# Kernel optimization log

Hardware: AMD Instinct MI355X
Metric: run time of the kernel (lower is better)

The kernel has to match this reference:

```python
import jax, jax.numpy as jnp
import numpy as np

RESO = 64            # plane_resolution
PADDING = 0.1
HID = 128            # hidden_dim
CDIM = 128           # c_dim
NBLOCKS = 5
PLANES = ((0, 2), (0, 1), (1, 2))  # xz, xy, yz column picks


def _plane_index(p, cols):
    # normalize_coordinate + coordinate2index (2d)
    xy = p[..., list(cols)] / (1.0 + PADDING + 1e-3) + 0.5
    xy = jnp.clip(xy, 0.0, 1.0 - 1e-3)
    ij = (xy * RESO).astype(jnp.int32)
    return ij[..., 0] + RESO * ij[..., 1]  # [B, T]


def _flat_idx(idx, S):
    B = idx.shape[0]
    return (idx + jnp.arange(B, dtype=idx.dtype)[:, None] * S).reshape(-1)


def _scatter_max(src, idx, S):
    # src [B,T,F], idx [B,T] -> [B,S,F]; empty bins -> 0 (torch_scatter convention)
    B, T, F = src.shape
    m = jax.ops.segment_max(src.reshape(B * T, F), _flat_idx(idx, S), num_segments=B * S)
    m = jnp.where(jnp.isfinite(m), m, jnp.zeros((), src.dtype))
    return m.reshape(B, S, F)


def _scatter_mean(src, idx, S):
    B, T, F = src.shape
    flat = _flat_idx(idx, S)
    s = jax.ops.segment_sum(src.reshape(B * T, F), flat, num_segments=B * S)
    cnt = jax.ops.segment_sum(jnp.ones((B * T,), src.dtype), flat, num_segments=B * S)
    return (s / jnp.maximum(cnt, 1.0)[:, None]).reshape(B, S, F)


def _resblock(x, w0, b0, w1, b1, ws):
    # ONet ResnetBlockFC: fc_1(relu(fc_0(relu(x)))) + shortcut(x)
    net = jax.nn.relu(x) @ w0 + b0
    dx = jax.nn.relu(net) @ w1 + b1
    return x @ ws + dx


def setup_inputs() -> dict:
    key = jax.random.key(0)
    ks = jax.random.split(key, 10)
    sc = 0.05
    return {
        "p": jax.random.normal(ks[0], (8, 20000, 3), dtype=jnp.float32),
        "fc_pos_w": jax.random.normal(ks[1], (3, 2 * HID), dtype=jnp.float32) * sc,
        "fc_pos_b": jnp.zeros((2 * HID,), jnp.float32),
        "blk0_w": jax.random.normal(ks[2], (NBLOCKS, 2 * HID, HID), dtype=jnp.float32) * sc,
        "blk0_b": jnp.zeros((NBLOCKS, HID), jnp.float32),
        "blk1_w": jax.random.normal(ks[3], (NBLOCKS, HID, HID), dtype=jnp.float32) * sc,
        "blk1_b": jnp.zeros((NBLOCKS, HID), jnp.float32),
        "blk_sc_w": jax.random.normal(ks[4], (NBLOCKS, 2 * HID, HID), dtype=jnp.float32) * sc,
        "fc_c_w": jax.random.normal(ks[5], (HID, CDIM), dtype=jnp.float32) * sc,
        "fc_c_b": jnp.zeros((CDIM,), jnp.float32),
    }


def reference(p, fc_pos_w, fc_pos_b, blk0_w, blk0_b, blk1_w, blk1_b, blk_sc_w, fc_c_w, fc_c_b):
    S = RESO * RESO
    B = p.shape[0]
    idxs = [_plane_index(p, cols) for cols in PLANES]

    net = p @ fc_pos_w + fc_pos_b                         # [B,T,2H]
    net = _resblock(net, blk0_w[0], blk0_b[0], blk1_w[0], blk1_b[0], blk_sc_w[0])
    for i in range(1, NBLOCKS):
        pooled = jnp.zeros_like(net[..., :HID])
        for idx in idxs:
            fea = _scatter_max(net, idx, S)               # [B,S,H]
            pooled = pooled + jnp.take_along_axis(fea, idx[:, :, None], axis=1)
        net = jnp.concatenate([net, pooled], axis=-1)     # [B,T,2H]
        net = _resblock(net, blk0_w[i], blk0_b[i], blk1_w[i], blk1_b[i], blk_sc_w[i])

    c = net @ fc_c_w + fc_c_b                             # [B,T,C]
    feas = []
    for idx in idxs:
        fp = _scatter_mean(c, idx, S)                     # [B,S,C]
        feas.append(fp.transpose(0, 2, 1).reshape(B, CDIM, RESO, RESO))
    return jnp.stack(feas)                                # [3,B,C,R,R] (xz, xy, yz)
```

## Files before the change

### kernel.cpp

```cpp
#include <hip/hip_runtime.h>
#include <cstdint>
#include <cstddef>

#define NP     160000
#define NB     8
#define TPB    20000
#define H      128
#define SS     4096
#define NCHUNK 625
#define NBLK   10
#define PPB    2000

typedef _Float16 half8  __attribute__((ext_vector_type(8)));
typedef _Float16 half4v __attribute__((ext_vector_type(4)));
typedef float    f32x16 __attribute__((ext_vector_type(16)));

__device__ __forceinline__ half8 reluh8(half8 x) {
  half8 z = (half8)(_Float16)0;
  return __builtin_elementwise_max(x, z);
}

__global__ __launch_bounds__(256) void k_idx(const float* __restrict__ p,
                                             int* __restrict__ idx) {
  int n = blockIdx.x * 256 + threadIdx.x;
  if (n >= NP) return;
  const float DEN = (float)(1.0 + 0.1 + 1e-3);
  const float HI  = (float)(1.0 - 1e-3);
  float px = p[3*n], py = p[3*n+1], pz = p[3*n+2];
  float nx = fminf(fmaxf(px / DEN + 0.5f, 0.0f), HI);
  float ny = fminf(fmaxf(py / DEN + 0.5f, 0.0f), HI);
  float nz = fminf(fmaxf(pz / DEN + 0.5f, 0.0f), HI);
  int ix = (int)(nx * 64.0f);
  int iy = (int)(ny * 64.0f);
  int iz = (int)(nz * 64.0f);
  idx[0*NP + n] = ix + 64 * iz;
  idx[1*NP + n] = ix + 64 * iy;
  idx[2*NP + n] = iy + 64 * iz;
}

__global__ __launch_bounds__(256) void k_hist(const int* __restrict__ idx,
                                              unsigned* __restrict__ hist) {
  __shared__ unsigned lh[SS];
  const int tid = threadIdx.x;
  const int plb = blockIdx.x % 24;
  const int blk = blockIdx.x / 24;
  const int pl = plb >> 3, b = plb & 7;
  for (int j = tid; j < SS; j += 256) lh[j] = 0;
  __syncthreads();
  const int base = pl*NP + b*TPB + blk*PPB;
  for (int j = tid; j < PPB; j += 256)
    atomicAdd(&lh[idx[base + j]], 1u);
  __syncthreads();
  unsigned* dst = hist + ((size_t)plb*NBLK + blk)*SS;
  for (int j = tid; j < SS; j += 256) dst[j] = lh[j];
}

__global__ __launch_bounds__(256) void k_scan2(unsigned* __restrict__ hist,
                                               unsigned* __restrict__ cnt,
                                               int* __restrict__ cursor) {
  __shared__ unsigned stot[SS];
  __shared__ unsigned ssum[256];
  __shared__ unsigned sbase[256];
  const int plb = blockIdx.x;
  const int tid = threadIdx.x;
  unsigned* hp = hist + (size_t)plb*NBLK*SS;
  for (int j = tid; j < SS; j += 256) {
    unsigned t = 0;
    #pragma unroll
    for (int blk = 0; blk < NBLK; ++blk) t += hp[blk*SS + j];
    stot[j] = t;
  }
  __syncthreads();
  unsigned local = 0;
  #pragma unroll
  for (int i = 0; i < 16; ++i) local += stot[tid*16 + i];
  ssum[tid] = local;
  __syncthreads();
  if (tid == 0) {
    unsigned run = 0;
    for (int i = 0; i < 256; ++i) { sbase[i] = run; run += ssum[i]; }
  }
  __syncthreads();
  unsigned run = sbase[tid];
  for (int i = 0; i < 16; ++i) {
    const int bin = tid*16 + i;
    const unsigned tot = stot[bin];
    cnt[plb*SS + bin] = tot;
    cursor[plb*SS + bin] = (int)(run + tot);
    unsigned acc = run;
    #pragma unroll
    for (int blk = 0; blk < NBLK; ++blk) {
      const unsigned c = hp[blk*SS + bin];
      hp[blk*SS + bin] = acc;
      acc += c;
    }
    run += tot;
  }
}

__global__ __launch_bounds__(256) void k_reorder2(const int* __restrict__ idx,
                                                  const unsigned* __restrict__ hist,
                                                  int* __restrict__ order) {
  __shared__ unsigned lrank[SS];
  const int tid = threadIdx.x;
  const int plb = blockIdx.x % 24;
  const int blk = blockIdx.x / 24;
  const int pl = plb >> 3, b = plb & 7;
  for (int j = tid; j < SS; j += 256) lrank[j] = 0;
  __syncthreads();
  const unsigned* bp = hist + ((size_t)plb*NBLK + blk)*SS;
  int* op = order + pl*NP + b*TPB;
  const int nbase = b*TPB + blk*PPB;
  for (int j = tid; j < PPB; j += 256) {
    const int n = nbase + j;
    const int bin = idx[pl*NP + n];
    const unsigned r = atomicAdd(&lrank[bin], 1u);
    op[bp[bin] + r] = (bin << 18) | n;
  }
}

__global__ __launch_bounds__(256) void k_wconv(const float* __restrict__ w0,
                                               const float* __restrict__ w1,
                                               const float* __restrict__ wsc,
                                               _Float16* __restrict__ wb) {
  int t = blockIdx.x*256 + threadIdx.x;
  if (t >= 51200) return;
  int L = t / 10240, r = t % 10240;
  const float* src; _Float16* dst; int q;
  if (r < 4096)      { q = r;        src = w0  + L*32768; dst = wb + L*81920;         }
  else if (r < 8192) { q = r - 4096; src = wsc + L*32768; dst = wb + L*81920 + 32768; }
  else               { q = r - 8192; src = w1  + L*16384; dst = wb + L*81920 + 65536; }
  int kt = q >> 8, nt = (q >> 6) & 3, l = q & 63;
  int k0 = kt*16 + ((l >> 5) << 3);
  int n  = nt*32 + (l & 31);
  union { _Float16 h[8]; uint4 u; } o;
  #pragma unroll
  for (int j = 0; j < 8; ++j) o.h[j] = (_Float16)src[(size_t)(k0 + j)*H + n];
  *(uint4*)(dst + (size_t)q*8) = o.u;
}

template<int OP>
__global__ __launch_bounds__(256) void k_poolA(const _Float16* __restrict__ net,
                                               const int* __restrict__ order,
                                               _Float16* __restrict__ fea,
                                               float* __restrict__ sums,
                                               float* __restrict__ pbufF,
                                               float* __restrict__ pbufL) {
  const int tid   = threadIdx.x;
  const int plb   = blockIdx.x % 24;
  const int chunk = (blockIdx.x / 24) * 8 + (tid >> 5);
  if (chunk >= NCHUNK) return;
  const int gi = tid & 31, f4 = gi << 2;
  const int pl = plb >> 3, b = plb & 7;
  const int base = pl*NP + b*TPB + chunk*32;
  const int pkv = order[base + gi];
  const int prevbin = (chunk > 0)          ? (order[base - 1] >> 18) : -1;
  const int nextbin = (chunk < NCHUNK - 1) ? (order[base + 32] >> 18) : -1;

  uint2 v[32];
  #pragma unroll
  for (int i = 0; i < 32; ++i) {
    const int pk = __shfl(pkv, i, 32);
    v[i] = *(const uint2*)&net[(size_t)(pk & 0x3FFFF)*H + f4];
  }
  __builtin_amdgcn_sched_barrier(0);

  const size_t pslot = ((size_t)plb*NCHUNK + chunk)*H + f4;
  int cur = __shfl(pkv, 0, 32) >> 18;
  int segstart = 0;
  float a0, a1, a2, a3;
  if (OP == 0) { a0 = a1 = a2 = a3 = -3.0e38f; } else { a0 = a1 = a2 = a3 = 0.f; }

  #pragma unroll
  for (int i = 0; i < 32; ++i) {
    const int bin = __shfl(pkv, i, 32) >> 18;
    if (bin != cur) {
      const bool contin = (segstart == 0) && (prevbin == cur);
      if (!contin) {
        if (OP == 0) {
          union { _Float16 h[4]; uint2 u; } o;
          o.h[0]=(_Float16)a0; o.h[1]=(_Float16)a1; o.h[2]=(_Float16)a2; o.h[3]=(_Float16)a3;
          *(uint2*)&fea[((size_t)plb*SS + cur)*H + f4] = o.u;
        } else {
          *(float4*)&sums[((size_t)plb*SS + cur)*H + f4] = make_float4(a0,a1,a2,a3);
        }
      } else {
        *(float4*)&pbufF[pslot] = make_float4(a0,a1,a2,a3);
      }
      cur = bin; segstart = i;
      if (OP == 0) { a0 = a1 = a2 = a3 = -3.0e38f; } else { a0 = a1 = a2 = a3 = 0.f; }
    }
    union { uint2 u; _Float16 h[4]; } w;
    w.u = v[i];
    if (OP == 0) {
      a0 = fmaxf(a0, (float)w.h[0]); a1 = fmaxf(a1, (float)w.h[1]);
      a2 = fmaxf(a2, (float)w.h[2]); a3 = fmaxf(a3, (float)w.h[3]);
    } else {
      a0 += (float)w.h[0]; a1 += (float)w.h[1];
      a2 += (float)w.h[2]; a3 += (float)w.h[3];
    }
  }
  const bool contin = (segstart == 0) && (prevbin == cur);
  const bool extend = (nextbin == cur);
  if (!contin && !extend) {
    if (OP == 0) {
      union { _Float16 h[4]; uint2 u; } o;
      o.h[0]=(_Float16)a0; o.h[1]=(_Float16)a1; o.h[2]=(_Float16)a2; o.h[3]=(_Float16)a3;
      *(uint2*)&fea[((size_t)plb*SS + cur)*H + f4] = o.u;
    } else {
      *(float4*)&sums[((size_t)plb*SS + cur)*H + f4] = make_float4(a0,a1,a2,a3);
    }
  } else if (contin) {
    *(float4*)&pbufF[pslot] = make_float4(a0,a1,a2,a3);
  } else {
    *(float4*)&pbufL[pslot] = make_float4(a0,a1,a2,a3);
  }
}

template<int OP>
__global__ __launch_bounds__(256) void k_poolB(const int* __restrict__ order,
                                               const int* __restrict__ cursor,
                                               _Float16* __restrict__ fea,
                                               float* __restrict__ sums,
                                               const float* __restrict__ pbufF,
                                               const float* __restrict__ pbufL) {
  const int tid = threadIdx.x;
  const int plb = blockIdx.x % 24;
  const int bnd = (blockIdx.x / 24) * 8 + (tid >> 5);
  if (bnd >= NCHUNK - 1) return;
  const int gi = tid & 31, f4 = gi << 2;
  const int pl = plb >> 3, b = plb & 7;
  const int base = pl*NP + b*TPB;
  const int pos  = (bnd + 1) * 32;
  const int binR = order[base + pos] >> 18;
  const int binL = order[base + pos - 1] >> 18;
  if (binL != binR) return;
  const int beta = binR;
  const int e = cursor[plb*SS + beta];
  const int s = (beta > 0) ? cursor[plb*SS + beta - 1] : 0;
  const int cs = s >> 5, ce = (e - 1) >> 5;
  if (cs != bnd) return;
  float4 acc = *(const float4*)&pbufL[((size_t)plb*NCHUNK + cs)*H + f4];
  #pragma unroll 4
  for (int c = cs + 1; c <= ce; ++c) {
    const float4 q = *(const float4*)&pbufF[((size_t)plb*NCHUNK + c)*H + f4];
    if (OP == 0) {
      acc.x = fmaxf(acc.x, q.x); acc.y = fmaxf(acc.y, q.y);
      acc.z = fmaxf(acc.z, q.z); acc.w = fmaxf(acc.w, q.w);
    } else {
      acc.x += q.x; acc.y += q.y; acc.z += q.z; acc.w += q.w;
    }
  }
  if (OP == 0) {
    union { _Float16 h[4]; uint2 u; } o;
    o.h[0]=(_Float16)acc.x; o.h[1]=(_Float16)acc.y;
    o.h[2]=(_Float16)acc.z; o.h[3]=(_Float16)acc.w;
    *(uint2*)&fea[((size_t)plb*SS + beta)*H + f4] = o.u;
  } else {
    *(float4*)&sums[((size_t)plb*SS + beta)*H + f4] = acc;
  }
}

template<int MODE>
__global__ __launch_bounds__(256, 4) void k_block(
    const float* __restrict__ p,
    const float* __restrict__ wpos, const float* __restrict__ bpos,
    _Float16* __restrict__ net,
    const _Float16* __restrict__ fea, const int* __restrict__ idx,
    const _Float16* __restrict__ wb,
    const float* __restrict__ b0, const float* __restrict__ b1)
{
  __shared__ char smem[32768];
  char* Xs = smem;
  char* Hs = smem;
  const int tid = threadIdx.x;
  const int n0  = blockIdx.x * 64;

  if (MODE == 0) {
    for (int j = tid; j < 64*64; j += 256) {
      int pt = j >> 6, k4 = (j & 63) << 2;
      int n = n0 + pt;
      float px = p[3*n], py = p[3*n+1], pz = p[3*n+2];
      float4 a  = *(const float4*)&bpos[k4];
      float4 wx = *(const float4*)&wpos[k4];
      float4 wy = *(const float4*)&wpos[256 + k4];
      float4 wz = *(const float4*)&wpos[512 + k4];
      a.x += px*wx.x + py*wy.x + pz*wz.x;
      a.y += px*wx.y + py*wy.y + pz*wz.y;
      a.z += px*wx.z + py*wy.z + pz*wz.z;
      a.w += px*wx.w + py*wy.w + pz*wz.w;
      union { _Float16 h[4]; uint2 u; } o;
      o.h[0] = (_Float16)a.x; o.h[1] = (_Float16)a.y;
      o.h[2] = (_Float16)a.z; o.h[3] = (_Float16)a.w;
      *(uint2*)(Xs + ((pt*512 + k4*2) ^ ((pt & 31) << 4))) = o.u;
    }
  } else {
    for (int j = tid; j < 64*32; j += 256) {
      int pt = j >> 5, k4 = (j & 31) << 2;
      int n = n0 + pt;
      int b = n / TPB;
      uint2 vleft = *(const uint2*)&net[(size_t)n*H + k4];
      union { uint2 u; half4v h; } w0g, w1g, w2g, o;
      w0g.u = *(const uint2*)&fea[(((size_t)(0*NB + b))*SS + idx[0*NP + n])*H + k4];
      w1g.u = *(const uint2*)&fea[(((size_t)(1*NB + b))*SS + idx[1*NP + n])*H + k4];
      w2g.u = *(const uint2*)&fea[(((size_t)(2*NB + b))*SS + idx[2*NP + n])*H + k4];
      o.h = (w0g.h + w1g.h) + w2g.h;
      const int sw = (pt & 31) << 4;
      *(uint2*)(Xs + ((pt*512 + k4*2) ^ sw)) = vleft;
      *(uint2*)(Xs + ((pt*512 + 256 + k4*2) ^ sw)) = o.u;
    }
  }
  __syncthreads();

  const int w  = tid >> 6;
  const int ln = tid & 63;
  const int l5 = ln >> 5;
  const int lr = ln & 31;
  const int sw = lr << 4;
  const int a0b = lr*512 + l5*16;
  const int a1b = a0b + 32*512;

  f32x16 aR0 = {}, aR1 = {}, aS0 = {}, aS1 = {};
  const _Float16* wb0 = wb;
  const _Float16* wbs = wb + 32768;

  #pragma unroll 4
  for (int kt = 0; kt < 16; ++kt) {
    half8 x0 = *(const half8*)(Xs + ((a0b + kt*32) ^ sw));
    half8 x1 = *(const half8*)(Xs + ((a1b + kt*32) ^ sw));
    half8 r0 = reluh8(x0);
    half8 r1 = reluh8(x1);
    half8 bw = *(const half8*)(wb0 + ((kt*4 + w)*64 + ln)*8);
    half8 bs = *(const half8*)(wbs + ((kt*4 + w)*64 + ln)*8);
    aR0 = __builtin_amdgcn_mfma_f32_32x32x16_f16(r0, bw, aR0, 0, 0, 0);
    aR1 = __builtin_amdgcn_mfma_f32_32x32x16_f16(r1, bw, aR1, 0, 0, 0);
    aS0 = __builtin_amdgcn_mfma_f32_32x32x16_f16(x0, bs, aS0, 0, 0, 0);
    aS1 = __builtin_amdgcn_mfma_f32_32x32x16_f16(x1, bs, aS1, 0, 0, 0);
  }
  __syncthreads();

  const int col = w*32 + lr;
  const float bb0 = b0[col];
  #pragma unroll
  for (int reg = 0; reg < 16; ++reg) {
    int ro = (reg & 3) + 8*(reg >> 2) + 4*l5;
    float v0 = fmaxf(aR0[reg] + bb0, 0.f);
    float v1 = fmaxf(aR1[reg] + bb0, 0.f);
    *(_Float16*)(Hs + ((ro*256 + col*2) ^ ((ro & 15) << 4)))      = (_Float16)v0;
    *(_Float16*)(Hs + (((32+ro)*256 + col*2) ^ ((ro & 15) << 4))) = (_Float16)v1;
  }
  __syncthreads();

  const _Float16* wb1 = wb + 65536;
  const int sw1 = (lr & 15) << 4;
  #pragma unroll 2
  for (int kt = 0; kt < 8; ++kt) {
    half8 h0 = *(const half8*)(Hs + ((lr*256 + l5*16 + kt*32) ^ sw1));
    half8 h1 = *(const half8*)(Hs + (((32+lr)*256 + l5*16 + kt*32) ^ sw1));
    half8 bf = *(const half8*)(wb1 + ((kt*4 + w)*64 + ln)*8);
    aS0 = __builtin_amdgcn_mfma_f32_32x32x16_f16(h0, bf, aS0, 0, 0, 0);
    aS1 = __builtin_amdgcn_mfma_f32_32x32x16_f16(h1, bf, aS1, 0, 0, 0);
  }

  const float bb1 = b1[col];
  #pragma unroll
  for (int reg = 0; reg < 16; ++reg) {
    int ro = (reg & 3) + 8*(reg >> 2) + 4*l5;
    net[(size_t)(n0 + ro)*H + col]      = (_Float16)(aS0[reg] + bb1);
    net[(size_t)(n0 + 32 + ro)*H + col] = (_Float16)(aS1[reg] + bb1);
  }
}

__global__ __launch_bounds__(256) void k_out2(const float* __restrict__ sums,
                                              const unsigned* __restrict__ cnt,
                                              const float* __restrict__ wc,
                                              const float* __restrict__ bc,
                                              float* __restrict__ out) {
  __shared__ float xa[64][132];
  const int plb = blockIdx.y;
  const int s0  = blockIdx.x << 6;
  const int tid = threadIdx.x;

  for (int j = tid; j < 64*32; j += 256) {
    int si = j >> 5, k4 = (j & 31) << 2;
    int s = s0 + si;
    float4 v = *(const float4*)&sums[((size_t)plb*SS + s)*H + k4];
    unsigned c = cnt[(size_t)plb*SS + s];
    float m = (c > 0u) ? (1.0f / (float)c) : 0.0f;
    xa[si][k4+0] = v.x*m; xa[si][k4+1] = v.y*m;
    xa[si][k4+2] = v.z*m; xa[si][k4+3] = v.w*m;
  }
  __syncthreads();

  const int fg = tid & 31;
  const int pg = tid >> 5;
  const int f4c = fg << 2;
  const int prow = pg << 3;
  float ac[8][4];
  #pragma unroll
  for (int i = 0; i < 8; ++i) { ac[i][0]=ac[i][1]=ac[i][2]=ac[i][3]=0.f; }
  #pragma unroll 4
  for (int k = 0; k < H; ++k) {
    const float4 wv = *(const float4*)&wc[(size_t)k*H + f4c];
    #pragma unroll
    for (int i = 0; i < 8; ++i) {
      const float xv = xa[prow + i][k];
      ac[i][0] += xv*wv.x; ac[i][1] += xv*wv.y; ac[i][2] += xv*wv.z; ac[i][3] += xv*wv.w;
    }
  }
  __syncthreads();
  const float4 bv = *(const float4*)&bc[f4c];
  #pragma unroll
  for (int i = 0; i < 8; ++i) {
    float4 o;
    o.x = ac[i][0] + bv.x;
    o.y = ac[i][1] + bv.y;
    o.z = ac[i][2] + bv.z;
    o.w = ac[i][3] + bv.w;
    *(float4*)&xa[prow + i][f4c] = o;
  }
  __syncthreads();

  for (int j = tid; j < H * 16; j += 256) {
    const int ch = j >> 4;
    const int s4 = (j & 15) << 2;
    float4 o;
    o.x = xa[s4 + 0][ch];
    o.y = xa[s4 + 1][ch];
    o.z = xa[s4 + 2][ch];
    o.w = xa[s4 + 3][ch];
    *(float4*)&out[((size_t)plb*H + ch)*SS + s0 + s4] = o;
  }
}

extern "C" void kernel_launch(void* const* d_in, const int* in_sizes, int n_in,
                              void* d_out, int out_size, void* d_ws, size_t ws_size,
                              hipStream_t stream) {
  (void)in_sizes; (void)n_in; (void)out_size; (void)ws_size;
  const float* p      = (const float*)d_in[0];
  const float* wpos   = (const float*)d_in[1];
  const float* bpos   = (const float*)d_in[2];
  const float* blk0w  = (const float*)d_in[3];
  const float* blk0b  = (const float*)d_in[4];
  const float* blk1w  = (const float*)d_in[5];
  const float* blk1b  = (const float*)d_in[6];
  const float* blkscw = (const float*)d_in[7];
  const float* wc     = (const float*)d_in[8];
  const float* bc     = (const float*)d_in[9];
  float* out = (float*)d_out;

  char* ws = (char*)d_ws;
  _Float16* net  = (_Float16*)ws;
  int* idx       = (int*)(ws + 40960000);
  int* order     = (int*)(ws + 42880000);
  int* cursor    = (int*)(ws + 44800000);
  unsigned* cnt  = (unsigned*)(ws + 45193216);
  _Float16* wb   = (_Float16*)(ws + 45586432);
  float* sums    = (float*)(ws + 46405632);
  float* pbufF   = (float*)(ws + 96737280);
  float* pbufL   = (float*)(ws + 104417280);
  unsigned* hist = (unsigned*)(ws + 112097280);
  _Float16* fea  = (_Float16*)d_out;

  k_idx<<<625, 256, 0, stream>>>(p, idx);
  k_hist<<<24*NBLK, 256, 0, stream>>>(idx, hist);
  k_scan2<<<24, 256, 0, stream>>>(hist, cnt, cursor);
  k_reorder2<<<24*NBLK, 256, 0, stream>>>(idx, hist, order);
  k_wconv<<<200, 256, 0, stream>>>(blk0w, blk1w, blkscw, wb);

  k_block<0><<<2500, 256, 0, stream>>>(p, wpos, bpos, net, nullptr, idx,
                                       wb, blk0b, blk1b);

  for (int i = 1; i < 5; ++i) {
    k_poolA<0><<<79*24, 256, 0, stream>>>(net, order, fea, nullptr, pbufF, pbufL);
    k_poolB<0><<<78*24, 256, 0, stream>>>(order, cursor, fea, nullptr, pbufF, pbufL);
    k_block<1><<<2500, 256, 0, stream>>>(nullptr, nullptr, nullptr, net, fea, idx,
                                         wb + (size_t)i*81920,
                                         blk0b + (size_t)i*H,
                                         blk1b + (size_t)i*H);
  }

  k_poolA<1><<<79*24, 256, 0, stream>>>(net, order, nullptr, sums, pbufF, pbufL);
  k_poolB<1><<<78*24, 256, 0, stream>>>(order, cursor, nullptr, sums, pbufF, pbufL);
  k_out2<<<dim3(64, 24), 256, 0, stream>>>(sums, cnt, wc, bc, out);
}
```

Before: 490.7 us.

## Fuse index computation into histogram and make block kernel persistent

The separate k_idx launch is removed. k_hist now computes each plane's bin index from the point coordinates, writes it out and counts it in the same pass. k_block switches to a grid-stride persistent loop over 64-point tiles with a fixed grid of 1024 blocks, and per-column biases and index constants are hoisted out of the tile loop. This saves one launch and block scheduling overhead, at the cost of a tail imbalance because 2500 tiles do not divide evenly across 1024 blocks, plus an extra barrier per tile.

```diff
diff --git a/kernel.cpp b/kernel.cpp
--- a/kernel.cpp
+++ b/kernel.cpp
@@ -10,6 +10,8 @@
 #define NCHUNK 625
 #define NBLK   10
 #define PPB    2000
+#define NTILE  2500
+#define GRIDP  1024
 
 typedef _Float16 half8  __attribute__((ext_vector_type(8)));
 typedef _Float16 half4v __attribute__((ext_vector_type(4)));
@@ -20,25 +22,8 @@
   return __builtin_elementwise_max(x, z);
 }
 
-__global__ __launch_bounds__(256) void k_idx(const float* __restrict__ p,
-                                             int* __restrict__ idx) {
-  int n = blockIdx.x * 256 + threadIdx.x;
-  if (n >= NP) return;
-  const float DEN = (float)(1.0 + 0.1 + 1e-3);
-  const float HI  = (float)(1.0 - 1e-3);
-  float px = p[3*n], py = p[3*n+1], pz = p[3*n+2];
-  float nx = fminf(fmaxf(px / DEN + 0.5f, 0.0f), HI);
-  float ny = fminf(fmaxf(py / DEN + 0.5f, 0.0f), HI);
-  float nz = fminf(fmaxf(pz / DEN + 0.5f, 0.0f), HI);
-  int ix = (int)(nx * 64.0f);
-  int iy = (int)(ny * 64.0f);
-  int iz = (int)(nz * 64.0f);
-  idx[0*NP + n] = ix + 64 * iz;
-  idx[1*NP + n] = ix + 64 * iy;
-  idx[2*NP + n] = iy + 64 * iz;
-}
-
-__global__ __launch_bounds__(256) void k_hist(const int* __restrict__ idx,
+__global__ __launch_bounds__(256) void k_hist(const float* __restrict__ p,
+                                              int* __restrict__ idx,
                                               unsigned* __restrict__ hist) {
   __shared__ unsigned lh[SS];
   const int tid = threadIdx.x;
@@ -47,9 +32,22 @@
   const int pl = plb >> 3, b = plb & 7;
   for (int j = tid; j < SS; j += 256) lh[j] = 0;
   __syncthreads();
-  const int base = pl*NP + b*TPB + blk*PPB;
-  for (int j = tid; j < PPB; j += 256)
-    atomicAdd(&lh[idx[base + j]], 1u);
+  const float DEN = (float)(1.0 + 0.1 + 1e-3);
+  const float HI  = (float)(1.0 - 1e-3);
+  const int nbase = b*TPB + blk*PPB;
+  for (int j = tid; j < PPB; j += 256) {
+    const int n = nbase + j;
+    const float px = p[3*n], py = p[3*n+1], pz = p[3*n+2];
+    float ca, cb;
+    if (pl == 0)      { ca = px; cb = pz; }
+    else if (pl == 1) { ca = px; cb = py; }
+    else              { ca = py; cb = pz; }
+    const float na = fminf(fmaxf(ca / DEN + 0.5f, 0.0f), HI);
+    const float nb = fminf(fmaxf(cb / DEN + 0.5f, 0.0f), HI);
+    const int bin = (int)(na * 64.0f) + 64 * (int)(nb * 64.0f);
+    idx[pl*NP + n] = bin;
+    atomicAdd(&lh[bin], 1u);
+  }
   __syncthreads();
   unsigned* dst = hist + ((size_t)plb*NBLK + blk)*SS;
   for (int j = tid; j < SS; j += 256) dst[j] = lh[j];
@@ -274,43 +272,6 @@
   char* Xs = smem;
   char* Hs = smem;
   const int tid = threadIdx.x;
-  const int n0  = blockIdx.x * 64;
-
-  if (MODE == 0) {
-    for (int j = tid; j < 64*64; j += 256) {
-      int pt = j >> 6, k4 = (j & 63) << 2;
-      int n = n0 + pt;
-      float px = p[3*n], py = p[3*n+1], pz = p[3*n+2];
-      float4 a  = *(const float4*)&bpos[k4];
-      float4 wx = *(const float4*)&wpos[k4];
-      float4 wy = *(const float4*)&wpos[256 + k4];
-      float4 wz = *(const float4*)&wpos[512 + k4];
-      a.x += px*wx.x + py*wy.x + pz*wz.x;
-      a.y += px*wx.y + py*wy.y + pz*wz.y;
-      a.z += px*wx.z + py*wy.z + pz*wz.z;
-      a.w += px*wx.w + py*wy.w + pz*wz.w;
-      union { _Float16 h[4]; uint2 u; } o;
-      o.h[0] = (_Float16)a.x; o.h[1] = (_Float16)a.y;
-      o.h[2] = (_Float16)a.z; o.h[3] = (_Float16)a.w;
-      *(uint2*)(Xs + ((pt*512 + k4*2) ^ ((pt & 31) << 4))) = o.u;
-    }
-  } else {
-    for (int j = tid; j < 64*32; j += 256) {
-      int pt = j >> 5, k4 = (j & 31) << 2;
-      int n = n0 + pt;
-      int b = n / TPB;
-      uint2 vleft = *(const uint2*)&net[(size_t)n*H + k4];
-      union { uint2 u; half4v h; } w0g, w1g, w2g, o;
-      w0g.u = *(const uint2*)&fea[(((size_t)(0*NB + b))*SS + idx[0*NP + n])*H + k4];
-      w1g.u = *(const uint2*)&fea[(((size_t)(1*NB + b))*SS + idx[1*NP + n])*H + k4];
-      w2g.u = *(const uint2*)&fea[(((size_t)(2*NB + b))*SS + idx[2*NP + n])*H + k4];
-      o.h = (w0g.h + w1g.h) + w2g.h;
-      const int sw = (pt & 31) << 4;
-      *(uint2*)(Xs + ((pt*512 + k4*2) ^ sw)) = vleft;
-      *(uint2*)(Xs + ((pt*512 + 256 + k4*2) ^ sw)) = o.u;
-    }
-  }
-  __syncthreads();
 
   const int w  = tid >> 6;
   const int ln = tid & 63;
@@ -319,55 +280,96 @@
   const int sw = lr << 4;
   const int a0b = lr*512 + l5*16;
   const int a1b = a0b + 32*512;
-
-  f32x16 aR0 = {}, aR1 = {}, aS0 = {}, aS1 = {};
+  const int col = w*32 + lr;
+  const int sw1 = (lr & 15) << 4;
+  const float bb0 = b0[col];
+  const float bb1 = b1[col];
   const _Float16* wb0 = wb;
   const _Float16* wbs = wb + 32768;
-
-  #pragma unroll 4
-  for (int kt = 0; kt < 16; ++kt) {
-    half8 x0 = *(const half8*)(Xs + ((a0b + kt*32) ^ sw));
-    half8 x1 = *(const half8*)(Xs + ((a1b + kt*32) ^ sw));
-    half8 r0 = reluh8(x0);
-    half8 r1 = reluh8(x1);
-    half8 bw = *(const half8*)(wb0 + ((kt*4 + w)*64 + ln)*8);
-    half8 bs = *(const half8*)(wbs + ((kt*4 + w)*64 + ln)*8);
-    aR0 = __builtin_amdgcn_mfma_f32_32x32x16_f16(r0, bw, aR0, 0, 0, 0);
-    aR1 = __builtin_amdgcn_mfma_f32_32x32x16_f16(r1, bw, aR1, 0, 0, 0);
-    aS0 = __builtin_amdgcn_mfma_f32_32x32x16_f16(x0, bs, aS0, 0, 0, 0);
-    aS1 = __builtin_amdgcn_mfma_f32_32x32x16_f16(x1, bs, aS1, 0, 0, 0);
-  }
-  __syncthreads();
-
-  const int col = w*32 + lr;
-  const float bb0 = b0[col];
-  #pragma unroll
-  for (int reg = 0; reg < 16; ++reg) {
-    int ro = (reg & 3) + 8*(reg >> 2) + 4*l5;
-    float v0 = fmaxf(aR0[reg] + bb0, 0.f);
-    float v1 = fmaxf(aR1[reg] + bb0, 0.f);
-    *(_Float16*)(Hs + ((ro*256 + col*2) ^ ((ro & 15) << 4)))      = (_Float16)v0;
-    *(_Float16*)(Hs + (((32+ro)*256 + col*2) ^ ((ro & 15) << 4))) = (_Float16)v1;
-  }
-  __syncthreads();
-
   const _Float16* wb1 = wb + 65536;
-  const int sw1 = (lr & 15) << 4;
-  #pragma unroll 2
-  for (int kt = 0; kt < 8; ++kt) {
-    half8 h0 = *(const half8*)(Hs + ((lr*256 + l5*16 + kt*32) ^ sw1));
-    half8 h1 = *(const half8*)(Hs + (((32+lr)*256 + l5*16 + kt*32) ^ sw1));
-    half8 bf = *(const half8*)(wb1 + ((kt*4 + w)*64 + ln)*8);
-    aS0 = __builtin_amdgcn_mfma_f32_32x32x16_f16(h0, bf, aS0, 0, 0, 0);
-    aS1 = __builtin_amdgcn_mfma_f32_32x32x16_f16(h1, bf, aS1, 0, 0, 0);
-  }
-
-  const float bb1 = b1[col];
-  #pragma unroll
-  for (int reg = 0; reg < 16; ++reg) {
-    int ro = (reg & 3) + 8*(reg >> 2) + 4*l5;
-    net[(size_t)(n0 + ro)*H + col]      = (_Float16)(aS0[reg] + bb1);
-    net[(size_t)(n0 + 32 + ro)*H + col] = (_Float16)(aS1[reg] + bb1);
+
+  for (int t = blockIdx.x; t < NTILE; t += gridDim.x) {
+    const int n0 = t * 64;
+    if (t != (int)blockIdx.x) __syncthreads();
+
+    if (MODE == 0) {
+      for (int j = tid; j < 64*64; j += 256) {
+        int pt = j >> 6, k4 = (j & 63) << 2;
+        int n = n0 + pt;
+        float px = p[3*n], py = p[3*n+1], pz = p[3*n+2];
+        float4 a  = *(const float4*)&bpos[k4];
+        float4 wx = *(const float4*)&wpos[k4];
+        float4 wy = *(const float4*)&wpos[256 + k4];
+        float4 wz = *(const float4*)&wpos[512 + k4];
+        a.x += px*wx.x + py*wy.x + pz*wz.x;
+        a.y += px*wx.y + py*wy.y + pz*wz.y;
+        a.z += px*wx.z + py*wy.z + pz*wz.z;
+        a.w += px*wx.w + py*wy.w + pz*wz.w;
+        union { _Float16 h[4]; uint2 u; } o;
+        o.h[0] = (_Float16)a.x; o.h[1] = (_Float16)a.y;
+        o.h[2] = (_Float16)a.z; o.h[3] = (_Float16)a.w;
+        *(uint2*)(Xs + ((pt*512 + k4*2) ^ ((pt & 31) << 4))) = o.u;
+      }
+    } else {
+      for (int j = tid; j < 64*32; j += 256) {
+        int pt = j >> 5, k4 = (j & 31) << 2;
+        int n = n0 + pt;
+        int b = n / TPB;
+        uint2 vleft = *(const uint2*)&net[(size_t)n*H + k4];
+        union { uint2 u; half4v h; } w0g, w1g, w2g, o;
+        w0g.u = *(const uint2*)&fea[(((size_t)(0*NB + b))*SS + idx[0*NP + n])*H + k4];
+        w1g.u = *(const uint2*)&fea[(((size_t)(1*NB + b))*SS + idx[1*NP + n])*H + k4];
+        w2g.u = *(const uint2*)&fea[(((size_t)(2*NB + b))*SS + idx[2*NP + n])*H + k4];
+        o.h = (w0g.h + w1g.h) + w2g.h;
+        const int swp = (pt & 31) << 4;
+        *(uint2*)(Xs + ((pt*512 + k4*2) ^ swp)) = vleft;
+        *(uint2*)(Xs + ((pt*512 + 256 + k4*2) ^ swp)) = o.u;
+      }
+    }
+    __syncthreads();
+
+    f32x16 aR0 = {}, aR1 = {}, aS0 = {}, aS1 = {};
+
+    #pragma unroll 4
+    for (int kt = 0; kt < 16; ++kt) {
+      half8 x0 = *(const half8*)(Xs + ((a0b + kt*32) ^ sw));
+      half8 x1 = *(const half8*)(Xs + ((a1b + kt*32) ^ sw));
+      half8 r0 = reluh8(x0);
+      half8 r1 = reluh8(x1);
+      half8 bw = *(const half8*)(wb0 + ((kt*4 + w)*64 + ln)*8);
+      half8 bs = *(const half8*)(wbs + ((kt*4 + w)*64 + ln)*8);
+      aR0 = __builtin_amdgcn_mfma_f32_32x32x16_f16(r0, bw, aR0, 0, 0, 0);
+      aR1 = __builtin_amdgcn_mfma_f32_32x32x16_f16(r1, bw, aR1, 0, 0, 0);
+      aS0 = __builtin_amdgcn_mfma_f32_32x32x16_f16(x0, bs, aS0, 0, 0, 0);
+      aS1 = __builtin_amdgcn_mfma_f32_32x32x16_f16(x1, bs, aS1, 0, 0, 0);
+    }
+    __syncthreads();
+
+    #pragma unroll
+    for (int reg = 0; reg < 16; ++reg) {
+      int ro = (reg & 3) + 8*(reg >> 2) + 4*l5;
+      float v0 = fmaxf(aR0[reg] + bb0, 0.f);
+      float v1 = fmaxf(aR1[reg] + bb0, 0.f);
+      *(_Float16*)(Hs + ((ro*256 + col*2) ^ ((ro & 15) << 4)))      = (_Float16)v0;
+      *(_Float16*)(Hs + (((32+ro)*256 + col*2) ^ ((ro & 15) << 4))) = (_Float16)v1;
+    }
+    __syncthreads();
+
+    #pragma unroll 2
+    for (int kt = 0; kt < 8; ++kt) {
+      half8 h0 = *(const half8*)(Hs + ((lr*256 + l5*16 + kt*32) ^ sw1));
+      half8 h1 = *(const half8*)(Hs + (((32+lr)*256 + l5*16 + kt*32) ^ sw1));
+      half8 bf = *(const half8*)(wb1 + ((kt*4 + w)*64 + ln)*8);
+      aS0 = __builtin_amdgcn_mfma_f32_32x32x16_f16(h0, bf, aS0, 0, 0, 0);
+      aS1 = __builtin_amdgcn_mfma_f32_32x32x16_f16(h1, bf, aS1, 0, 0, 0);
+    }
+
+    #pragma unroll
+    for (int reg = 0; reg < 16; ++reg) {
+      int ro = (reg & 3) + 8*(reg >> 2) + 4*l5;
+      net[(size_t)(n0 + ro)*H + col]      = (_Float16)(aS0[reg] + bb1);
+      net[(size_t)(n0 + 32 + ro)*H + col] = (_Float16)(aS1[reg] + bb1);
+    }
   }
 }
 
@@ -462,22 +464,21 @@
   unsigned* hist = (unsigned*)(ws + 112097280);
   _Float16* fea  = (_Float16*)d_out;
 
-  k_idx<<<625, 256, 0, stream>>>(p, idx);
-  k_hist<<<24*NBLK, 256, 0, stream>>>(idx, hist);
+  k_hist<<<24*NBLK, 256, 0, stream>>>(p, idx, hist);
   k_scan2<<<24, 256, 0, stream>>>(hist, cnt, cursor);
   k_reorder2<<<24*NBLK, 256, 0, stream>>>(idx, hist, order);
   k_wconv<<<200, 256, 0, stream>>>(blk0w, blk1w, blkscw, wb);
 
-  k_block<0><<<2500, 256, 0, stream>>>(p, wpos, bpos, net, nullptr, idx,
-                                       wb, blk0b, blk1b);
+  k_block<0><<<GRIDP, 256, 0, stream>>>(p, wpos, bpos, net, nullptr, idx,
+                                        wb, blk0b, blk1b);
 
   for (int i = 1; i < 5; ++i) {
     k_poolA<0><<<79*24, 256, 0, stream>>>(net, order, fea, nullptr, pbufF, pbufL);
     k_poolB<0><<<78*24, 256, 0, stream>>>(order, cursor, fea, nullptr, pbufF, pbufL);
-    k_block<1><<<2500, 256, 0, stream>>>(nullptr, nullptr, nullptr, net, fea, idx,
-                                         wb + (size_t)i*81920,
-                                         blk0b + (size_t)i*H,
-                                         blk1b + (size_t)i*H);
+    k_block<1><<<GRIDP, 256, 0, stream>>>(nullptr, nullptr, nullptr, net, fea, idx,
+                                          wb + (size_t)i*81920,
+                                          blk0b + (size_t)i*H,
+                                          blk1b + (size_t)i*H);
   }
 
   k_poolA<1><<<79*24, 256, 0, stream>>>(net, order, nullptr, sums, pbufF, pbufL);
```

Result: slower. 519.5 us (+5.9%).
